# Performance work log

Hardware: AMD Instinct MI355X
Metric: run time of the kernel (lower is better)

## Reference

```python
import jax, jax.numpy as jnp
import numpy as np

C = 256      # nlevels (channels); SphereConv filters == nlevels
NLAT = 256   # latitudes == number of l modes (L)
NLON = 512   # longitudes
L = NLAT
M = NLON // 2 + 1  # rfft modes (m)
NREF = L // 4      # interval=4 reference points for filter interpolation
EPS = 1e-3         # keras GroupNormalization default epsilon


def setup_inputs() -> dict:
    key = jax.random.key(0)
    ks = jax.random.split(key, 16)
    s = 1.0 / np.sqrt(C)
    return {
        "x": jax.random.normal(ks[0], (C, NLAT, NLON), dtype=jnp.float32),
        "legfuncs": jax.random.normal(ks[1], (L, M, NLAT), dtype=jnp.float32) / np.sqrt(NLAT),
        "wquad": jax.random.uniform(ks[2], (NLAT,), dtype=jnp.float32),
        "w_real": jax.random.normal(ks[3], (C, C, NREF), dtype=jnp.float32),
        "w_imag": jax.random.normal(ks[4], (C, C, NREF), dtype=jnp.float32),
        "m1w1": jax.random.normal(ks[5], (C, C), dtype=jnp.float32) * s,
        "m1b1": jnp.zeros((C,), dtype=jnp.float32),
        "m1w2": jax.random.normal(ks[6], (C, C), dtype=jnp.float32) * s,
        "m1b2": jnp.zeros((C,), dtype=jnp.float32),
        "m2w1": jax.random.normal(ks[7], (C, C), dtype=jnp.float32) * s,
        "m2b1": jnp.zeros((C,), dtype=jnp.float32),
        "m2w2": jax.random.normal(ks[8], (C, C), dtype=jnp.float32) * s,
        "m2b2": jnp.zeros((C,), dtype=jnp.float32),
        "gamma": jnp.ones((C,), dtype=jnp.float32),
        "beta": jnp.zeros((C,), dtype=jnp.float32),
    }


def _gelu(v):
    return jax.nn.gelu(v, approximate=False)  # tf.nn.gelu / keras 'gelu' default is exact erf form


def _interp_filters(w, Lout):
    # tfp.math.interp_regular_1d_grid: linear interp of (F, C, NREF) along last axis
    # onto Lout targets spanning [0, Lout-1] mapped to the NREF-point ref grid.
    n = w.shape[-1]
    pos = jnp.arange(Lout, dtype=jnp.float32) * (n - 1) / (Lout - 1)
    i0 = jnp.clip(jnp.floor(pos).astype(jnp.int32), 0, n - 2)
    frac = pos - i0.astype(jnp.float32)
    return w[..., i0] * (1.0 - frac) + w[..., i0 + 1] * frac  # (F, C, Lout)


def reference(x, legfuncs, wquad, w_real, w_imag,
              m1w1, m1b1, m1w2, m1b2,
              m2w1, m2b1, m2w2, m2b2, gamma, beta):
    Cc = x.shape[0]
    Ll = legfuncs.shape[0]
    # --- grid_obj.calc_sh_coeffs: rfft over lon + weighted Legendre transform over lat ---
    F = jnp.fft.rfft(x, axis=-1)                                   # (C, nlat, M) complex64
    lw = (legfuncs * wquad[None, None, :]).astype(jnp.complex64)   # (L, M, nlat)
    harms = jnp.einsum('lmj,cjm->clm', lw, F)                      # (C, L, M)
    # --- SphereConv: interpolate complex filters, mean over channels, scale by sqrt(1+l) ---
    Wr = _interp_filters(w_real, Ll)
    Wi = _interp_filters(w_imag, Ll)
    W = jax.lax.complex(Wr, Wi)                                    # (F, C, L)
    lfac = jnp.sqrt(1.0 + jnp.arange(Ll, dtype=jnp.float32))       # self.l
    xs = jnp.einsum('fcl,clm->flm', W, harms) / Cc * lfac[:, None] # mean over axis -3
    # --- grid_obj.eval: inverse Legendre + irfft ---
    G = jnp.einsum('lmj,flm->fjm', legfuncs.astype(jnp.complex64), xs)  # (F, nlat, M)
    grids = jnp.fft.irfft(G, n=x.shape[-1], axis=-1)               # (F, nlat, nlon) real
    grids = _gelu(grids)
    g = jnp.transpose(grids, (2, 1, 0))                            # (nlon, nlat, F)
    # --- MLP1(x^T) + spectral branch ---
    x1 = jnp.transpose(x, (2, 1, 0))                               # (nlon, nlat, C)
    h1 = _gelu(x1 @ m1w1 + m1b1)
    y1 = _gelu(h1 @ m1w2 + m1b2)
    added = y1 + g
    # --- MLP2 with instance norm (GroupNormalization groups=-1, eps=1e-3) ---
    h2 = _gelu(added @ m2w1 + m2b1)
    y2 = _gelu(h2 @ m2w2 + m2b2)
    mu = jnp.mean(y2, axis=(0, 1), keepdims=True)
    var = jnp.var(y2, axis=(0, 1), keepdims=True)
    yn = (y2 - mu) * jax.lax.rsqrt(var + EPS) * gamma + beta
    out = jnp.transpose(yn, (2, 1, 0))                             # (C, nlat, nlon)
    return out + x
```

## Files before the change

### kernel.cpp

```cpp
#include <hip/hip_runtime.h>


typedef __bf16 bf16x8 __attribute__((ext_vector_type(8)));
typedef float f32x4 __attribute__((ext_vector_type(4)));
typedef unsigned short u16;
typedef unsigned int u32;

__device__ __forceinline__ u16 f2b(float f){
  u32 u = __float_as_uint(f);
  u32 r = (u + 0x7FFFu + ((u >> 16) & 1u)) >> 16;
  return (u16)r;
}
__device__ __forceinline__ float b2f(u16 h){
  return __uint_as_float(((u32)h) << 16);
}
__device__ __forceinline__ float gelu_fast(float v){
  float u2 = v * (1.5957691216057308f + 0.07135481627260025f * v * v);
  float e  = __expf(-u2);
  return v * __builtin_amdgcn_rcpf(1.0f + e);
}


__global__ __launch_bounds__(256) void k_ftab(u16* Tc, u16* Ts){
  int i = blockIdx.x*256 + threadIdx.x;
  if (i >= 384*512) return;
  int m = i >> 9, n = i & 511;
  if (m >= 257){ Tc[i]=0; Ts[i]=0; return; }
  int r = (m*n) & 511;
  float th = (float)r * (6.283185307179586f/512.0f);
  Tc[i] = f2b(cosf(th));
  Ts[i] = f2b(-sinf(th));
}
__global__ __launch_bounds__(256) void k_itab(u16* tr, u16* ti){
  int i = blockIdx.x*256 + threadIdx.x;
  if (i >= 512*288) return;
  int n = i / 288, m = i % 288;
  if (m >= 257){ tr[i]=0; ti[i]=0; return; }
  int r = (n*m) & 511;
  float th = (float)r * (6.283185307179586f/512.0f);
  float cm = (m==0 || m==256) ? (1.0f/512.0f) : (2.0f/512.0f);
  tr[i] = f2b(cm*cosf(th));
  ti[i] = f2b(-cm*sinf(th));
}
__global__ __launch_bounds__(256) void k_lw(const float* __restrict__ leg,
                                            const float* __restrict__ wq,
                                            u16* __restrict__ lw, int total8){
  int i = blockIdx.x*256 + threadIdx.x;
  if (i >= total8) return;
  long long base = (long long)i * 8;
  float4 a = *(const float4*)(leg + base);
  float4 b = *(const float4*)(leg + base + 4);
  int j = (int)(base & 255);
  u16 o[8];
  o[0]=f2b(a.x*wq[j  ]); o[1]=f2b(a.y*wq[j+1]); o[2]=f2b(a.z*wq[j+2]); o[3]=f2b(a.w*wq[j+3]);
  o[4]=f2b(b.x*wq[j+4]); o[5]=f2b(b.y*wq[j+5]); o[6]=f2b(b.z*wq[j+6]); o[7]=f2b(b.w*wq[j+7]);
  *(uint4*)(lw + base) = *(const uint4*)o;
}
__global__ __launch_bounds__(256) void k_xprep(const float* __restrict__ x,
                                               u16* __restrict__ xT, u16* __restrict__ x_bf){
  __shared__ u16 tile[64*64];
  const int j = blockIdx.z;
  const int n0 = blockIdx.x*64, c0 = blockIdx.y*64;
  const int t = threadIdx.x;
  #pragma unroll
  for (int r = 0; r < 4; r++){
    int idx = r*256 + t;
    int cl = idx >> 4;
    int n4 = (idx & 15) * 4;
    long long off = ((long long)(c0+cl))*131072 + (long long)j*512 + n0 + n4;
    float4 v = *(const float4*)(x + off);
    u16 b[4] = { f2b(v.x), f2b(v.y), f2b(v.z), f2b(v.w) };
    *(unsigned long long*)(x_bf + off) = *(const unsigned long long*)b;
    int sw = ((n4 >> 2) & 7) << 3;
    tile[(n4+0)*64 + (cl ^ sw)] = b[0];
    tile[(n4+1)*64 + (cl ^ sw)] = b[1];
    tile[(n4+2)*64 + (cl ^ sw)] = b[2];
    tile[(n4+3)*64 + (cl ^ sw)] = b[3];
  }
  __syncthreads();
  #pragma unroll
  for (int r = 0; r < 2; r++){
    int idx = r*256 + t;
    int nl = idx >> 3;
    int cq = (idx & 7) * 8;
    uint4 v = *(const uint4*)&tile[nl*64 + (cq ^ (((nl>>2)&7)<<3))];
    *(uint4*)(xT + ((long long)(n0+nl))*65536 + (long long)j*256 + c0 + cq) = v;
  }
}
__global__ __launch_bounds__(256) void k_legT(const float* __restrict__ leg,
                                              u16* __restrict__ legT){
  __shared__ u16 tile[64*64];
  const int m = blockIdx.z;
  const int l0 = blockIdx.x*64, j0 = blockIdx.y*64;
  const int t = threadIdx.x;
  #pragma unroll
  for (int r = 0; r < 4; r++){
    int idx = r*256 + t;
    int ll = idx >> 4;
    int j4 = (idx & 15) * 4;
    float4 v = *(const float4*)(leg + ((long long)(l0+ll))*65792 + (long long)m*256 + j0 + j4);
    u16 b[4] = { f2b(v.x), f2b(v.y), f2b(v.z), f2b(v.w) };
    int sw = ((j4 >> 2) & 7) << 3;
    tile[(j4+0)*64 + (ll ^ sw)] = b[0];
    tile[(j4+1)*64 + (ll ^ sw)] = b[1];
    tile[(j4+2)*64 + (ll ^ sw)] = b[2];
    tile[(j4+3)*64 + (ll ^ sw)] = b[3];
  }
  __syncthreads();
  #pragma unroll
  for (int r = 0; r < 2; r++){
    int idx = r*256 + t;
    int jl = idx >> 3;
    int lq = (idx & 7) * 8;
    uint4 v = *(const uint4*)&tile[jl*64 + (lq ^ (((jl>>2)&7)<<3))];
    *(uint4*)(legT + (long long)m*65536 + (long long)(j0+jl)*256 + l0 + lq) = v;
  }
}

__global__ __launch_bounds__(256)
void tr_f32b(const float* __restrict__ src, u16* __restrict__ dst,
             int R, int Cc, long long ir, long long ib, long long oc, long long ob){
  __shared__ float tile[32][33];
  const long long b = blockIdx.z;
  const int r0 = blockIdx.y*32, c0 = blockIdx.x*32;
  const int tx = threadIdx.x & 31, ty = threadIdx.x >> 5;
  const float* s = src + b*ib;
  #pragma unroll
  for (int rr = ty; rr < 32; rr += 8){
    int r = r0 + rr, c = c0 + tx;
    float v = 0.0f;
    if (r < R && c < Cc) v = s[(long long)r*ir + c];
    tile[rr][tx] = v;
  }
  __syncthreads();
  u16* d = dst + b*ob;
  #pragma unroll
  for (int cc = ty; cc < 32; cc += 8){
    int c = c0 + cc, r = r0 + tx;
    if (r < R && c < Cc) d[(long long)c*oc + r] = f2b(tile[tx][cc]);
  }
}
__global__ __launch_bounds__(256)
void tr_b16(const u16* __restrict__ src, u16* __restrict__ dst,
            int R, int Rpad, int Cc, long long ir, long long ib, long long oc, long long ob){
  __shared__ u16 tile[32][34];
  const long long b = blockIdx.z;
  const int r0 = blockIdx.y*32, c0 = blockIdx.x*32;
  const int tx = threadIdx.x & 31, ty = threadIdx.x >> 5;
  const u16* s = src + b*ib;
  #pragma unroll
  for (int rr = ty; rr < 32; rr += 8){
    int r = r0 + rr, c = c0 + tx;
    tile[rr][tx] = (r < R && c < Cc) ? s[(long long)r*ir + c] : (u16)0;
  }
  __syncthreads();
  u16* d = dst + b*ob;
  #pragma unroll
  for (int cc = ty; cc < 32; cc += 8){
    int c = c0 + cc, r = r0 + tx;
    if (r < Rpad && c < Cc) d[(long long)c*oc + r] = tile[tx][cc];
  }
}

__global__ __launch_bounds__(256) void k_interp(const float* __restrict__ wr,
                                                const float* __restrict__ wi,
                                                u16* __restrict__ Wr2, u16* __restrict__ Wi2){
  __shared__ float sr[64][65], si[64][65];
  const int f = blockIdx.x;
  const int c0 = blockIdx.y * 64;
  const float* gr = wr + ((long long)f*256 + c0)*64;
  const float* gi = wi + ((long long)f*256 + c0)*64;
  for (int t = threadIdx.x*4; t < 4096; t += 1024){
    float4 vr = *(const float4*)(gr + t);
    float4 vi = *(const float4*)(gi + t);
    int cc = t >> 6, k = t & 63;
    sr[cc][k]=vr.x; sr[cc][k+1]=vr.y; sr[cc][k+2]=vr.z; sr[cc][k+3]=vr.w;
    si[cc][k]=vi.x; si[cc][k+1]=vi.y; si[cc][k+2]=vi.z; si[cc][k+3]=vi.w;
  }
  __syncthreads();
  const int lane_c = threadIdx.x & 63;
  const int lgrp = threadIdx.x >> 6;
  for (int l = lgrp; l < 256; l += 4){
    float pos = (float)l * (63.0f/255.0f);
    int i0 = min((int)pos, 62);
    float fr = pos - (float)i0;
    float s = sqrtf(1.0f + (float)l) * (1.0f/256.0f);
    long long o = (long long)l*65536 + f*256 + c0 + lane_c;
    Wr2[o] = f2b((sr[lane_c][i0]*(1.0f-fr) + sr[lane_c][i0+1]*fr)*s);
    Wi2[o] = f2b((si[lane_c][i0]*(1.0f-fr) + si[lane_c][i0+1]*fr)*s);
  }
}

struct GemmP {
  const u16 *A0, *A1, *B0, *B1;
  u16 *C0, *C1;
  const float *bias;
  const u16 *addsrc;
  int M, Mout, N, K;
  int lda, ldb, ldc;
  long long bsA, bsB, bsC;
};

__device__ __forceinline__ void gl2lds16(const u16* g, u16* l){
  __builtin_amdgcn_global_load_lds(
      (const __attribute__((address_space(1))) u32*)((const void*)g),
      (__attribute__((address_space(3))) u32*)((void*)l),
      16, 0, 0);
}

__device__ __forceinline__ void stage_slow(u16* sT, const u16* g, long long ld,
                                           int row0, int rmax, int k0, int K, int tid){
  #pragma unroll
  for (int h = 0; h < 2; h++){
    int s = tid + h*256;
    int row = s >> 2;
    int col = (((s & 3) ^ ((s >> 3) & 3)) << 3);
    int grow = row0 + row;
    u16 v[8];
    #pragma unroll
    for (int e = 0; e < 8; e++){
      int gc = k0 + col + e;
      v[e] = (grow < rmax && gc < K) ? g[(long long)grow*ld + gc] : (u16)0;
    }
    *(uint4*)(sT + s*8) = *(const uint4*)v;
  }
}

template<int MODE, int EPI>
__global__ __launch_bounds__(256, (MODE==0) ? 4 : 2)
void g128(GemmP p){
  constexpr int NA = (MODE==0 || MODE==2) ? 1 : 2;
  constexpr int NB = (MODE==0 || MODE==3) ? 1 : 2;
  constexpr bool DUAL = (MODE >= 2);
  __shared__ u16 sA[NA][4096];
  __shared__ u16 sB[NB][4096];

  const int tid = threadIdx.x;
  const long long bz = blockIdx.z;
  const int row0 = blockIdx.y*128, col0 = blockIdx.x*128;
  const int lane = tid & 63, wid = tid >> 6;
  const int wr = wid >> 1, wc = wid & 1;
  const int quad = lane >> 4, l15 = lane & 15;

  const u16* Ag[NA]; const u16* Bg[NB];
  Ag[0] = p.A0 + bz*p.bsA;
  if (NA == 2) Ag[1] = p.A1 + bz*p.bsA;
  Bg[0] = p.B0 + bz*p.bsB;
  if (NB == 2) Bg[1] = p.B1 + bz*p.bsB;

  const int srow = tid >> 2;
  const int scol = (((tid & 3) ^ ((tid >> 3) & 3)) << 3);
  const bool fA = (row0 + 128 <= p.M);
  const bool fB = (col0 + 128 <= p.N);

  int aoff[4], boff[4];
  #pragma unroll
  for (int i=0;i<4;i++){
    int ar = wr*64 + i*16 + l15;
    aoff[i] = ar*32 + ((quad ^ ((ar>>1)&3))<<3);
    int br = wc*64 + i*16 + l15;
    boff[i] = br*32 + ((quad ^ ((br>>1)&3))<<3);
  }

  f32x4 acc0[4][4], acc1[4][4];
  #pragma unroll
  for (int i=0;i<4;i++)
    #pragma unroll
    for (int j=0;j<4;j++){
      acc0[i][j] = (f32x4){0.f,0.f,0.f,0.f};
      if (DUAL) acc1[i][j] = (f32x4){0.f,0.f,0.f,0.f};
    }

  for (int k0 = 0; k0 < p.K; k0 += 32){
    __syncthreads();
    const bool fk = (k0 + 32 <= p.K);
    #pragma unroll
    for (int t=0;t<NA;t++){
      if (fA && fk){
        const u16* g = Ag[t] + (long long)(row0 + srow)*p.lda + scol + k0;
        gl2lds16(g, &sA[t][tid*8]);
        gl2lds16(g + 64LL*p.lda, &sA[t][tid*8 + 2048]);
      } else stage_slow(&sA[t][0], Ag[t], p.lda, row0, p.M, k0, p.K, tid);
    }
    #pragma unroll
    for (int t=0;t<NB;t++){
      if (fB && fk){
        const u16* g = Bg[t] + (long long)(col0 + srow)*p.ldb + scol + k0;
        gl2lds16(g, &sB[t][tid*8]);
        gl2lds16(g + 64LL*p.ldb, &sB[t][tid*8 + 2048]);
      } else stage_slow(&sB[t][0], Bg[t], p.ldb, col0, p.N, k0, p.K, tid);
    }
    __syncthreads();

    bf16x8 a[NA][4], b[NB][4];
    #pragma unroll
    for (int t=0;t<NA;t++)
      #pragma unroll
      for (int i=0;i<4;i++) a[t][i] = *(const bf16x8*)&sA[t][aoff[i]];
    #pragma unroll
    for (int t=0;t<NB;t++)
      #pragma unroll
      for (int i=0;i<4;i++) b[t][i] = *(const bf16x8*)&sB[t][boff[i]];

    bf16x8 an[4];
    if (MODE == 4){
      #pragma unroll
      for (int i=0;i<4;i++){
        an[i] = a[1][i];
        u32* u = (u32*)&an[i];
        #pragma unroll
        for (int r=0;r<4;r++) u[r] ^= 0x80008000u;
      }
    }

    #pragma unroll
    for (int i=0;i<4;i++){
      #pragma unroll
      for (int j=0;j<4;j++){
        if (MODE == 0){
          acc0[i][j] = __builtin_amdgcn_mfma_f32_16x16x32_bf16(a[0][i], b[0][j], acc0[i][j], 0,0,0);
        } else if (MODE == 1){
          acc0[i][j] = __builtin_amdgcn_mfma_f32_16x16x32_bf16(a[0][i], b[0][j], acc0[i][j], 0,0,0);
          acc0[i][j] = __builtin_amdgcn_mfma_f32_16x16x32_bf16(a[1][i], b[1][j], acc0[i][j], 0,0,0);
        } else if (MODE == 2){
          acc0[i][j] = __builtin_amdgcn_mfma_f32_16x16x32_bf16(a[0][i], b[0][j], acc0[i][j], 0,0,0);
          acc1[i][j] = __builtin_amdgcn_mfma_f32_16x16x32_bf16(a[0][i], b[1][j], acc1[i][j], 0,0,0);
        } else if (MODE == 3){
          acc0[i][j] = __builtin_amdgcn_mfma_f32_16x16x32_bf16(a[0][i], b[0][j], acc0[i][j], 0,0,0);
          acc1[i][j] = __builtin_amdgcn_mfma_f32_16x16x32_bf16(a[1][i], b[0][j], acc1[i][j], 0,0,0);
        } else {
          acc0[i][j] = __builtin_amdgcn_mfma_f32_16x16x32_bf16(a[0][i], b[0][j], acc0[i][j], 0,0,0);
          acc0[i][j] = __builtin_amdgcn_mfma_f32_16x16x32_bf16(an[i],   b[1][j], acc0[i][j], 0,0,0);
          acc1[i][j] = __builtin_amdgcn_mfma_f32_16x16x32_bf16(a[0][i], b[1][j], acc1[i][j], 0,0,0);
          acc1[i][j] = __builtin_amdgcn_mfma_f32_16x16x32_bf16(a[1][i], b[0][j], acc1[i][j], 0,0,0);
        }
      }
    }
  }

  const long long cb = bz * p.bsC;
  #pragma unroll
  for (int i=0;i<4;i++){
    const int gr0 = row0 + wr*64 + i*16 + quad*4;
    #pragma unroll
    for (int j=0;j<4;j++){
      const int gc = col0 + wc*64 + j*16 + l15;
      if (gc >= p.N) continue;
      const float bval = (EPI==2 || EPI==3) ? p.bias[gc] : 0.0f;
      #pragma unroll
      for (int r=0;r<4;r++){
        const int gr = gr0 + r;
        if (gr >= p.Mout) continue;
        const long long ci = cb + (long long)gr * p.ldc + gc;
        float v = acc0[i][j][r];
        if (EPI==0){
          p.C0[ci] = f2b(v);
          if (DUAL) p.C1[ci] = f2b(acc1[i][j][r]);
        }
        else if (EPI==1) p.C0[ci] = f2b(gelu_fast(v));
        else if (EPI==2) p.C0[ci] = f2b(gelu_fast(v + bval));
        else             p.C0[ci] = f2b(gelu_fast(v + bval) + b2f(p.addsrc[ci]));
      }
    }
  }
}

__global__ __launch_bounds__(256) void k_red(const u16* __restrict__ y2,
                                             float* __restrict__ gs, float* __restrict__ gss){
  __shared__ float ls[8][260], lss[8][260];
  const int t = threadIdx.x;
  const int cb = (t & 31) * 8;
  const int rg = t >> 5;
  long long row0 = (long long)blockIdx.x * 256 + rg;
  float s[8], q[8];
  #pragma unroll
  for (int e=0;e<8;e++){ s[e]=0.f; q[e]=0.f; }
  for (int k = 0; k < 32; k++){
    uint4 v = *(const uint4*)(y2 + (row0 + (long long)k*8)*256 + cb);
    const u16* pv = (const u16*)&v;
    #pragma unroll
    for (int e=0;e<8;e++){ float f = b2f(pv[e]); s[e]+=f; q[e]+=f*f; }
  }
  #pragma unroll
  for (int e=0;e<8;e++){ ls[rg][cb+e]=s[e]; lss[rg][cb+e]=q[e]; }
  __syncthreads();
  float S = 0.f, Q = 0.f;
  #pragma unroll
  for (int g=0; g<8; g++){ S += ls[g][t]; Q += lss[g][t]; }
  atomicAdd(&gs[t], S);
  atomicAdd(&gss[t], Q);
}
__global__ __launch_bounds__(256) void k_out(const u16* __restrict__ y2, const float* __restrict__ x,
                                             const float* __restrict__ gs, const float* __restrict__ gss,
                                             const float* __restrict__ gamma, const float* __restrict__ beta,
                                             float* __restrict__ out){
  __shared__ float tile[64*64];
  __shared__ float sa[64], sb2[64];
  const int j = blockIdx.z;
  const int n0 = blockIdx.x*64, c0 = blockIdx.y*64;
  const int t = threadIdx.x;
  if (t < 64){
    int c = c0 + t;
    float mu = gs[c]*(1.0f/131072.0f);
    float var = gss[c]*(1.0f/131072.0f) - mu*mu;
    float a = rsqrtf(var + 1e-3f)*gamma[c];
    sa[t] = a; sb2[t] = beta[c] - mu*a;
  }
  #pragma unroll
  for (int r = 0; r < 2; r++){
    int idx = r*256 + t;
    int nl = idx >> 3, cq = (idx & 7)*8;
    uint4 v = *(const uint4*)(y2 + ((long long)(n0+nl))*65536 + (long long)j*256 + c0 + cq);
    const u16* pv = (const u16*)&v;
    #pragma unroll
    for (int e=0;e<8;e++){
      int c = cq + e;
      tile[c*64 + (nl ^ (c & 0x38))] = b2f(pv[e]);
    }
  }
  __syncthreads();
  #pragma unroll
  for (int r = 0; r < 4; r++){
    int idx = r*256 + t;
    int cl = idx >> 4, nq = (idx & 15)*4;
    float4 w = *(const float4*)&tile[cl*64 + (nq ^ (cl & 0x38))];
    float a = sa[cl], b = sb2[cl];
    long long oi = ((long long)(c0+cl))*131072 + (long long)j*512 + n0 + nq;
    float4 xv = *(const float4*)(x + oi);
    float4 o;
    o.x = w.x*a + b + xv.x;
    o.y = w.y*a + b + xv.y;
    o.z = w.z*a + b + xv.z;
    o.w = w.w*a + b + xv.w;
    *(float4*)(out + oi) = o;
  }
}

extern "C" void kernel_launch(void* const* d_in, const int* in_sizes, int n_in,
                              void* d_out, int out_size, void* d_ws, size_t ws_size,
                              hipStream_t stream){
  (void)in_sizes; (void)n_in; (void)out_size; (void)ws_size;
  const float* x     = (const float*)d_in[0];
  const float* legf  = (const float*)d_in[1];
  const float* wq    = (const float*)d_in[2];
  const float* w_r   = (const float*)d_in[3];
  const float* w_i   = (const float*)d_in[4];
  const float* m1w1  = (const float*)d_in[5];
  const float* m1b1  = (const float*)d_in[6];
  const float* m1w2  = (const float*)d_in[7];
  const float* m1b2  = (const float*)d_in[8];
  const float* m2w1  = (const float*)d_in[9];
  const float* m2b1  = (const float*)d_in[10];
  const float* m2w2  = (const float*)d_in[11];
  const float* m2b2  = (const float*)d_in[12];
  const float* gamma = (const float*)d_in[13];
  const float* beta  = (const float*)d_in[14];

  char* ws = (char*)d_ws;
  const size_t SZ_SA = 67108864ULL;
  const size_t SZ_SB = 67371008ULL;
  const size_t SZ_SC = 69206016ULL;
  const size_t SZ_SD = 75497472ULL;
  char* F  = ws;
  char* SA = ws + 4194304ULL;
  char* SB = SA + SZ_SA;
  char* SC = SB + SZ_SB;
  char* SD = SC + SZ_SC;

  u16* Tc   = (u16*)(F + 0x000000);
  u16* Ts   = (u16*)(F + 0x060000);
  u16* tabr = (u16*)(F + 0x0C0000);
  u16* tabi = (u16*)(F + 0x108000);
  u16* w1t  = (u16*)(F + 0x150000);
  u16* w2t  = (u16*)(F + 0x170000);
  u16* w3t  = (u16*)(F + 0x190000);
  u16* w4t  = (u16*)(F + 0x1B0000);
  float* gsum = (float*)(F + 0x1D0000);
  float* gssq = (float*)(F + 0x1D0400);

  const size_t HS = 33685504ULL;
  u16* xT   = (u16*)SA;
  u16* x_bf = (u16*)SB;
  u16* lw   = (u16*)SC;
  u16* Fr2  = (u16*)SD;
  u16* Fi2  = (u16*)(SD + HS);
  u16* hr3  = (u16*)SB;
  u16* hi3  = (u16*)(SB + HS);
  u16* Wr2  = (u16*)SD;
  u16* Wi2  = (u16*)(SD + HS);
  u16* xs3r = (u16*)SC;
  u16* xs3i = (u16*)(SC + 34603008ULL);
  u16* legT = (u16*)SB;
  u16* xs4r = (u16*)SD;
  u16* xs4i = (u16*)(SD + HS);
  u16* Gr5  = (u16*)SC;
  u16* Gi5  = (u16*)(SC + HS);
  u16* Gr6  = (u16*)SD;
  u16* Gi6  = (u16*)(SD + 37748736ULL);
  u16* g6   = (u16*)SB;
  u16* h1   = (u16*)SD;
  u16* addb = (u16*)SA;
  u16* h2   = (u16*)SD;
  u16* y2   = (u16*)SB;

  k_ftab<<<dim3(768), dim3(256), 0, stream>>>(Tc, Ts);
  k_itab<<<dim3(576), dim3(256), 0, stream>>>(tabr, tabi);
  tr_f32b<<<dim3(8,8,1), dim3(256), 0, stream>>>(m1w1, w1t, 256,256, 256,0, 256,0);
  tr_f32b<<<dim3(8,8,1), dim3(256), 0, stream>>>(m1w2, w2t, 256,256, 256,0, 256,0);
  tr_f32b<<<dim3(8,8,1), dim3(256), 0, stream>>>(m2w1, w3t, 256,256, 256,0, 256,0);
  tr_f32b<<<dim3(8,8,1), dim3(256), 0, stream>>>(m2w2, w4t, 256,256, 256,0, 256,0);
  k_xprep<<<dim3(8,4,256), dim3(256), 0, stream>>>(x, xT, x_bf);
  k_lw<<<dim3(8224), dim3(256), 0, stream>>>(legf, wq, lw, 2105344);

  {
    GemmP p{Tc, Ts, x_bf, nullptr, Fr2, Fi2, nullptr, nullptr,
            384, 257, 65536, 512, 512, 512, 65536, 0, 0, 0};
    g128<3,0><<<dim3(512,3,1), dim3(256), 0, stream>>>(p);
  }
  {
    GemmP p{lw, nullptr, Fr2, Fi2, hr3, hi3, nullptr, nullptr,
            256, 256, 256, 256, 65792, 256, 256, 256, 65536, 65536};
    g128<2,0><<<dim3(2,2,257), dim3(256), 0, stream>>>(p);
  }
  k_interp<<<dim3(256,4), dim3(256), 0, stream>>>(w_r, w_i, Wr2, Wi2);
  {
    GemmP p{Wr2, Wi2, hr3, hi3, xs3r, xs3i, nullptr, nullptr,
            256, 256, 257, 256, 256, 65536, 264, 65536, 256, 67584};
    g128<4,0><<<dim3(3,2,256), dim3(256), 0, stream>>>(p);
  }
  k_legT<<<dim3(4,4,257), dim3(256), 0, stream>>>(legf, legT);
  tr_b16<<<dim3(9,8,256), dim3(256), 0, stream>>>(xs3r, xs4r, 256,256,257, 67584,264, 65536,256);
  tr_b16<<<dim3(9,8,256), dim3(256), 0, stream>>>(xs3i, xs4i, 256,256,257, 67584,264, 65536,256);
  {
    GemmP p{xs4r, xs4i, legT, nullptr, Gr5, Gi5, nullptr, nullptr,
            256, 256, 256, 256, 256, 256, 256, 65536, 65536, 65536};
    g128<3,0><<<dim3(2,2,257), dim3(256), 0, stream>>>(p);
  }
  tr_b16<<<dim3(8,9,256), dim3(256), 0, stream>>>(Gr5, Gr6, 257,288,256, 65536,256, 73728,288);
  tr_b16<<<dim3(8,9,256), dim3(256), 0, stream>>>(Gi5, Gi6, 257,288,256, 65536,256, 73728,288);
  {
    GemmP p{tabr, tabi, Gr6, Gi6, g6, nullptr, nullptr, nullptr,
            512, 512, 65536, 288, 288, 288, 65536, 0, 0, 0};
    g128<1,1><<<dim3(512,4,1), dim3(256), 0, stream>>>(p);
  }
  {
    GemmP p{xT, nullptr, w1t, nullptr, h1, nullptr, m1b1, nullptr,
            131072, 131072, 256, 256, 256, 256, 256, 0, 0, 0};
    g128<0,2><<<dim3(2,1024,1), dim3(256), 0, stream>>>(p);
    p.A0 = h1; p.B0 = w2t; p.C0 = addb; p.bias = m1b2; p.addsrc = g6;
    g128<0,3><<<dim3(2,1024,1), dim3(256), 0, stream>>>(p);
  }
  {
    GemmP p{addb, nullptr, w3t, nullptr, h2, nullptr, m2b1, nullptr,
            131072, 131072, 256, 256, 256, 256, 256, 0, 0, 0};
    g128<0,2><<<dim3(2,1024,1), dim3(256), 0, stream>>>(p);
    p.A0 = h2; p.B0 = w4t; p.C0 = y2; p.bias = m2b2;
    g128<0,2><<<dim3(2,1024,1), dim3(256), 0, stream>>>(p);
  }
  hipMemsetAsync(gsum, 0, 2048, stream);
  k_red<<<dim3(512), dim3(256), 0, stream>>>(y2, gsum, gssq);
  k_out<<<dim3(8,4,256), dim3(256), 0, stream>>>(y2, x, gsum, gssq, gamma, beta, (float*)d_out);
}
```

Before: 1.175 ms.

## Fuse four MLP GEMMs into one kernel keeping activations in LDS

The four per-layer GEMM launches (MLP1 and MLP2, each with GELU and bias epilogues plus the residual add of the spectral branch) are replaced by one kernel. Each block takes 64 rows, keeps the intermediate 64x256 bf16 activations in swizzled LDS, and streams the weight matrices through LDS in k-slices. The goal is to remove the global write and read of three 131072x256 intermediate tensors and three launches. In exchange, each block reloads all four weight matrices, tiles are smaller (64 rows), and LDS use of about 52KB limits occupancy.

```diff
diff --git a/kernel.cpp b/kernel.cpp
--- a/kernel.cpp
+++ b/kernel.cpp
@@ -346,7 +346,6 @@
     for (int j=0;j<4;j++){
       const int gc = col0 + wc*64 + j*16 + l15;
       if (gc >= p.N) continue;
-      const float bval = (EPI==2 || EPI==3) ? p.bias[gc] : 0.0f;
       #pragma unroll
       for (int r=0;r<4;r++){
         const int gr = gr0 + r;
@@ -357,11 +356,141 @@
           p.C0[ci] = f2b(v);
           if (DUAL) p.C1[ci] = f2b(acc1[i][j][r]);
         }
-        else if (EPI==1) p.C0[ci] = f2b(gelu_fast(v));
-        else if (EPI==2) p.C0[ci] = f2b(gelu_fast(v + bval));
-        else             p.C0[ci] = f2b(gelu_fast(v + bval) + b2f(p.addsrc[ci]));
+        else p.C0[ci] = f2b(gelu_fast(v));
       }
     }
+  }
+}
+
+struct MlpP {
+  const u16 *A, *W1, *W2, *W3, *W4, *g6;
+  const float *B1, *B2, *B3, *B4;
+  u16 *y2;
+};
+
+__device__ __forceinline__ void zacc(f32x4 (&acc)[4][4]){
+  #pragma unroll
+  for (int i=0;i<4;i++)
+    #pragma unroll
+    for (int j=0;j<4;j++) acc[i][j] = (f32x4){0.f,0.f,0.f,0.f};
+}
+
+__device__ __forceinline__ void gemm_h(const u16* __restrict__ W, u16* sB, const u16* hL,
+                                       f32x4 (&acc)[4][4], int tid, int quad, int l15,
+                                       const int* boff){
+  for (int k0 = 0; k0 < 256; k0 += 32){
+    __syncthreads();
+    #pragma unroll
+    for (int h=0;h<4;h++){
+      int s = tid + h*256;
+      int sc = (((s & 3) ^ ((s >> 3) & 3)) << 3);
+      gl2lds16(W + (long long)(s>>2)*256 + sc + k0, &sB[s*8]);
+    }
+    __syncthreads();
+    bf16x8 a[4], b[4];
+    const int kg = k0 >> 3;
+    #pragma unroll
+    for (int i=0;i<4;i++){
+      int ar = i*16 + l15;
+      a[i] = *(const bf16x8*)&hL[ar*256 + (((kg + quad) ^ (ar & 31)) << 3)];
+    }
+    #pragma unroll
+    for (int j=0;j<4;j++) b[j] = *(const bf16x8*)&sB[boff[j]];
+    #pragma unroll
+    for (int i=0;i<4;i++)
+      #pragma unroll
+      for (int j=0;j<4;j++)
+        acc[i][j] = __builtin_amdgcn_mfma_f32_16x16x32_bf16(a[i], b[j], acc[i][j], 0,0,0);
+  }
+}
+
+template<bool ADD>
+__device__ __forceinline__ void epi_lds(f32x4 (&acc)[4][4], const float* __restrict__ bias,
+                                        u16* hL, const u16* __restrict__ add, long long r0,
+                                        int wid, int quad, int l15){
+  #pragma unroll
+  for (int j=0;j<4;j++){
+    const int col = wid*64 + j*16 + l15;
+    const float bv = bias[col];
+    const int cg = col >> 3, cl = col & 7;
+    #pragma unroll
+    for (int i=0;i<4;i++){
+      #pragma unroll
+      for (int r=0;r<4;r++){
+        const int row = i*16 + quad*4 + r;
+        float v = gelu_fast(acc[i][j][r] + bv);
+        if (ADD) v += b2f(add[(r0+row)*256 + col]);
+        hL[row*256 + (((cg ^ (row & 31)) << 3) | cl)] = f2b(v);
+      }
+    }
+  }
+}
+
+__global__ __launch_bounds__(256, 3) void f_mlp(MlpP p){
+  __shared__ u16 sA[2048];
+  __shared__ u16 sB[8192];
+  __shared__ u16 hL[16384];
+  const int tid = threadIdx.x;
+  const long long r0 = (long long)blockIdx.x * 64;
+  const int lane = tid & 63, wid = tid >> 6;
+  const int quad = lane >> 4, l15 = lane & 15;
+
+  int aoff[4], boff[4];
+  #pragma unroll
+  for (int i=0;i<4;i++){
+    int ar = i*16 + l15;
+    aoff[i] = ar*32 + ((quad ^ ((ar>>1)&3))<<3);
+    int br = wid*64 + i*16 + l15;
+    boff[i] = br*32 + ((quad ^ ((br>>1)&3))<<3);
+  }
+  const int sacol = (((tid & 3) ^ ((tid >> 3) & 3)) << 3);
+
+  f32x4 acc[4][4];
+  zacc(acc);
+  for (int k0 = 0; k0 < 256; k0 += 32){
+    __syncthreads();
+    gl2lds16(p.A + (r0 + (tid>>2))*256 + sacol + k0, &sA[tid*8]);
+    #pragma unroll
+    for (int h=0;h<4;h++){
+      int s = tid + h*256;
+      int sc = (((s & 3) ^ ((s >> 3) & 3)) << 3);
+      gl2lds16(p.W1 + (long long)(s>>2)*256 + sc + k0, &sB[s*8]);
+    }
+    __syncthreads();
+    bf16x8 a[4], b[4];
+    #pragma unroll
+    for (int i=0;i<4;i++) a[i] = *(const bf16x8*)&sA[aoff[i]];
+    #pragma unroll
+    for (int j=0;j<4;j++) b[j] = *(const bf16x8*)&sB[boff[j]];
+    #pragma unroll
+    for (int i=0;i<4;i++)
+      #pragma unroll
+      for (int j=0;j<4;j++)
+        acc[i][j] = __builtin_amdgcn_mfma_f32_16x16x32_bf16(a[i], b[j], acc[i][j], 0,0,0);
+  }
+  epi_lds<false>(acc, p.B1, hL, nullptr, r0, wid, quad, l15);
+
+  zacc(acc);
+  gemm_h(p.W2, sB, hL, acc, tid, quad, l15, boff);
+  __syncthreads();
+  epi_lds<true>(acc, p.B2, hL, p.g6, r0, wid, quad, l15);
+
+  zacc(acc);
+  gemm_h(p.W3, sB, hL, acc, tid, quad, l15, boff);
+  __syncthreads();
+  epi_lds<false>(acc, p.B3, hL, nullptr, r0, wid, quad, l15);
+
+  zacc(acc);
+  gemm_h(p.W4, sB, hL, acc, tid, quad, l15, boff);
+  __syncthreads();
+  epi_lds<false>(acc, p.B4, hL, nullptr, r0, wid, quad, l15);
+  __syncthreads();
+  #pragma unroll
+  for (int pass=0;pass<8;pass++){
+    int row = pass*8 + (tid>>5);
+    int g = tid & 31;
+    uint4 v = *(const uint4*)&hL[row*256 + (((g ^ (row & 31)) << 3))];
+    *(uint4*)(p.y2 + (r0+row)*256 + g*8) = v;
   }
 }
 
@@ -498,10 +627,7 @@
   u16* Gr6  = (u16*)SD;
   u16* Gi6  = (u16*)(SD + 37748736ULL);
   u16* g6   = (u16*)SB;
-  u16* h1   = (u16*)SD;
-  u16* addb = (u16*)SA;
-  u16* h2   = (u16*)SD;
-  u16* y2   = (u16*)SB;
+  u16* y2   = (u16*)SD;
 
   k_ftab<<<dim3(768), dim3(256), 0, stream>>>(Tc, Ts);
   k_itab<<<dim3(576), dim3(256), 0, stream>>>(tabr, tabi);
@@ -544,18 +670,8 @@
     g128<1,1><<<dim3(512,4,1), dim3(256), 0, stream>>>(p);
   }
   {
-    GemmP p{xT, nullptr, w1t, nullptr, h1, nullptr, m1b1, nullptr,
-            131072, 131072, 256, 256, 256, 256, 256, 0, 0, 0};
-    g128<0,2><<<dim3(2,1024,1), dim3(256), 0, stream>>>(p);
-    p.A0 = h1; p.B0 = w2t; p.C0 = addb; p.bias = m1b2; p.addsrc = g6;
-    g128<0,3><<<dim3(2,1024,1), dim3(256), 0, stream>>>(p);
-  }
-  {
-    GemmP p{addb, nullptr, w3t, nullptr, h2, nullptr, m2b1, nullptr,
-            131072, 131072, 256, 256, 256, 256, 256, 0, 0, 0};
-    g128<0,2><<<dim3(2,1024,1), dim3(256), 0, stream>>>(p);
-    p.A0 = h2; p.B0 = w4t; p.C0 = y2; p.bias = m2b2;
-    g128<0,2><<<dim3(2,1024,1), dim3(256), 0, stream>>>(p);
+    MlpP mp{xT, w1t, w2t, w3t, w4t, g6, m1b1, m1b2, m2b1, m2b2, y2};
+    f_mlp<<<dim3(2048), dim3(256), 0, stream>>>(mp);
   }
   hipMemsetAsync(gsum, 0, 2048, stream);
   k_red<<<dim3(512), dim3(256), 0, stream>>>(y2, gsum, gssq);
```

After: 1.193 ms. No clear change (+1.5%).
